# Performance work log

Hardware: AMD Instinct MI355X
Metric: run time of the kernel (lower is better)

The kernel has to match this reference:

```python
import jax, jax.numpy as jnp
import numpy as np

L = 4        # num_layers
B = 32       # batch
N = 512      # num_nodes == seq_len
D = 256      # d_model
H = 8        # nhead
HD = D // H  # head_dim
F = 1024     # dim_feedforward
EPS = 1e-5


def setup_inputs() -> dict:
    key = jax.random.key(0)
    ks = jax.random.split(key, 12)
    w = lambda k, shape: jax.random.normal(k, shape, jnp.float32) * 0.02
    return {
        "src": jax.random.normal(ks[0], (B, N, D), jnp.float32),
        # node embeddings (torch.randn -> std 1)
        "e1": jax.random.normal(ks[1], (N, D), jnp.float32),
        "e2": jax.random.normal(ks[2], (N, D), jnp.float32),
        # per-layer attention projections, stored [L, d_in, d_out]
        "Wq": w(ks[3], (L, D, D)), "bq": jnp.zeros((L, D), jnp.float32),
        "Wk": w(ks[4], (L, D, D)), "bk": jnp.zeros((L, D), jnp.float32),
        "Wv": w(ks[5], (L, D, D)), "bv": jnp.zeros((L, D), jnp.float32),
        "Wo": w(ks[6], (L, D, D)), "bo": jnp.zeros((L, D), jnp.float32),
        # FFN
        "W1": w(ks[7], (L, D, F)), "b1": jnp.zeros((L, F), jnp.float32),
        "W2": w(ks[8], (L, F, D)), "b2": jnp.zeros((L, D), jnp.float32),
        # LayerNorms
        "g1": jnp.ones((L, D), jnp.float32), "be1": jnp.zeros((L, D), jnp.float32),
        "g2": jnp.ones((L, D), jnp.float32), "be2": jnp.zeros((L, D), jnp.float32),
    }


def _layernorm(x, g, b):
    mu = jnp.mean(x, axis=-1, keepdims=True)
    var = jnp.mean(jnp.square(x - mu), axis=-1, keepdims=True)
    return (x - mu) * jax.lax.rsqrt(var + EPS) * g + b


def reference(src, e1, e2, Wq, bq, Wk, bk, Wv, bv, Wo, bo,
              W1, b1, W2, b2, g1, be1, g2, be2):
    # adaptive spatial bias shared across all layers: [N, N]
    bias = jnp.matmul(e1, e2.T)
    scale = 1.0 / jnp.sqrt(jnp.float32(HD))
    x = src
    for l in range(L):
        def heads(t):  # [B,N,D] -> [B,H,N,HD]
            return t.reshape(B, N, H, HD).transpose(0, 2, 1, 3)
        q = heads(x @ Wq[l] + bq[l])
        k = heads(x @ Wk[l] + bk[l])
        v = heads(x @ Wv[l] + bv[l])
        # scores + shared additive bias (broadcast over batch and heads)
        scores = jnp.einsum('bhqd,bhkd->bhqk', q, k) * scale + bias
        attn = jax.nn.softmax(scores, axis=-1)
        o = jnp.einsum('bhqk,bhkd->bhqd', attn, v)
        o = o.transpose(0, 2, 1, 3).reshape(B, N, D) @ Wo[l] + bo[l]
        x = _layernorm(x + o, g1[l], be1[l])
        ff = jax.nn.relu(x @ W1[l] + b1[l]) @ W2[l] + b2[l]
        x = _layernorm(x + ff, g2[l], be2[l])
    return x
```

## Files before the change

kernel.cpp:

```cpp
#include <hip/hip_runtime.h>

typedef __bf16 bf16;
typedef __bf16 v4bf __attribute__((ext_vector_type(4)));
typedef __bf16 v8bf __attribute__((ext_vector_type(8)));
typedef float  v4f  __attribute__((ext_vector_type(4)));
typedef float  v16f __attribute__((ext_vector_type(16)));
typedef unsigned short u16;
typedef u16 v8us __attribute__((ext_vector_type(8)));
typedef unsigned int v4u __attribute__((ext_vector_type(4)));
typedef _Float16 f16;
typedef f16 v4h __attribute__((ext_vector_type(4)));

#define L_ 4
#define B_ 32
#define N_ 512
#define D_ 256
#define H_ 8
#define F_ 1024
#define ROWS (B_*N_)
#define QHSZ ((size_t)B_*H_*N_*32)

__device__ __forceinline__ void gload16(const void* g, void* l) {
  __builtin_amdgcn_global_load_lds((__attribute__((address_space(1))) void*)g,
                                   (__attribute__((address_space(3))) void*)l,
                                   16, 0, 0);
}

__device__ __forceinline__ unsigned pk_bf16(float a, float b) {
  unsigned r;
  asm("v_cvt_pk_bf16_f32 %0, %1, %2" : "=v"(r) : "v"(a), "v"(b));
  return r;
}

#define PLSWAP(a, b) asm volatile("v_permlane32_swap_b32 %0, %1" : "+v"(a), "+v"(b))

#define EXP2(x) __builtin_amdgcn_exp2f(x)

__device__ __forceinline__ unsigned encf(float f) {
  unsigned u = __float_as_uint(f);
  return (u & 0x80000000u) ? ~u : (u | 0x80000000u);
}
__device__ __forceinline__ float decf(unsigned e) {
  unsigned b = (e & 0x80000000u) ? (e & 0x7fffffffu) : ~e;
  return __uint_as_float(b);
}

template <int N> __device__ __forceinline__ void waitvm() {
  if constexpr (N == 0) asm volatile("s_waitcnt vmcnt(0)" ::: "memory");
  else if constexpr (N == 2) asm volatile("s_waitcnt vmcnt(2)" ::: "memory");
  else if constexpr (N == 3) asm volatile("s_waitcnt vmcnt(3)" ::: "memory");
  else if constexpr (N == 4) asm volatile("s_waitcnt vmcnt(4)" ::: "memory");
  else if constexpr (N == 5) asm volatile("s_waitcnt vmcnt(5)" ::: "memory");
  else if constexpr (N == 6) asm volatile("s_waitcnt vmcnt(6)" ::: "memory");
}

__global__ __launch_bounds__(256) void bias_gemm(
    const float* __restrict__ eK, const float* __restrict__ eQ,
    float* __restrict__ biasP, unsigned* __restrict__ mqe) {
  __shared__ float As[32][17];
  __shared__ float Bs[32][17];
  __shared__ float pm[16][32];
  const int tx = threadIdx.x, ty = threadIdx.y;
  const int t = ty * 16 + tx;
  const int lrow = t >> 3, lkq = (t & 7) * 2;
  const int r0 = blockIdx.y * 32, c0 = blockIdx.x * 32;
  float acc[2][2] = {{0.f, 0.f}, {0.f, 0.f}};
  for (int k0 = 0; k0 < D_; k0 += 16) {
    const float2 a2 = *(const float2*)&eK[(size_t)(r0 + lrow) * D_ + k0 + lkq];
    const float2 b2 = *(const float2*)&eQ[(size_t)(c0 + lrow) * D_ + k0 + lkq];
    As[lrow][lkq] = a2.x; As[lrow][lkq + 1] = a2.y;
    Bs[lrow][lkq] = b2.x; Bs[lrow][lkq + 1] = b2.y;
    __syncthreads();
#pragma unroll
    for (int k = 0; k < 16; ++k) {
      const float a0 = As[ty * 2][k], a1 = As[ty * 2 + 1][k];
      const float b0 = Bs[tx * 2][k], b1 = Bs[tx * 2 + 1][k];
      acc[0][0] += a0 * b0; acc[0][1] += a0 * b1;
      acc[1][0] += a1 * b0; acc[1][1] += a1 * b1;
    }
    __syncthreads();
  }
#pragma unroll
  for (int i = 0; i < 2; ++i)
#pragma unroll
    for (int j = 0; j < 2; ++j) acc[i][j] *= 1.4426950408889634f;
#pragma unroll
  for (int i = 0; i < 2; ++i) {
    const int gr = r0 + ty * 2 + i;
    const int kb = gr >> 5, r5 = gr & 31;
    const int blk = kb * 8 + (r5 >> 3) * 2 + ((r5 >> 2) & 1);
#pragma unroll
    for (int j = 0; j < 2; ++j) {
      const int q = c0 + tx * 2 + j;
      biasP[(size_t)(blk * 512 + q) * 4 + (r5 & 3)] = acc[i][j];
    }
  }
  pm[ty][tx * 2]     = fmaxf(acc[0][0], acc[1][0]);
  pm[ty][tx * 2 + 1] = fmaxf(acc[0][1], acc[1][1]);
  __syncthreads();
  if (ty == 0) {
#pragma unroll
    for (int j = 0; j < 2; ++j) {
      float m = pm[0][tx * 2 + j];
#pragma unroll
      for (int y = 1; y < 16; ++y) m = fmaxf(m, pm[y][tx * 2 + j]);
      atomicMax(&mqe[c0 + tx * 2 + j], encf(m));
    }
  }
}

__device__ __forceinline__ void convT_tile(
    const float* __restrict__ W, bf16* __restrict__ Wt,
    int K, int N, size_t inL, size_t outL, int l, int k0, int n0, int tid,
    float (*t)[33]) {
  const int r = tid >> 5, c = tid & 31;
#pragma unroll
  for (int i = 0; i < 4; ++i)
    t[r + 8 * i][c] = W[l * inL + (size_t)(k0 + r + 8 * i) * N + n0 + c];
  __syncthreads();
#pragma unroll
  for (int i = 0; i < 4; ++i)
    Wt[l * outL + (size_t)(n0 + r + 8 * i) * K + k0 + c] = (bf16)t[c][r + 8 * i];
}

__global__ __launch_bounds__(256) void setup_all(
    const float* __restrict__ src, bf16* __restrict__ xb,
    const float* __restrict__ bq, const float* __restrict__ bk,
    const float* __restrict__ bv, float* __restrict__ bqkv,
    const float* __restrict__ Wq, const float* __restrict__ Wk,
    const float* __restrict__ Wv, const float* __restrict__ Wo,
    const float* __restrict__ W1, const float* __restrict__ W2,
    bf16* __restrict__ Wqkvt, bf16* __restrict__ Wot,
    bf16* __restrict__ W1t, bf16* __restrict__ W2t,
    const float* __restrict__ biasP, f16* __restrict__ biasH,
    const unsigned* __restrict__ mqe) {
  __shared__ float t[32][33];
  const int tid = threadIdx.x;
  int id = blockIdx.x;
  if (id < 4096) {
    const int i = id * 256 + tid;
    float4 v = ((const float4*)src)[i];
    uint2 w;
    w.x = pk_bf16(v.x, v.y);
    w.y = pk_bf16(v.z, v.w);
    ((uint2*)xb)[i] = w;
    return;
  }
  id -= 4096;
  if (id < 12) {
    const int i = id * 256 + tid;
    if (i < L_ * 768) {
      const int l = i / 768, n = i - l * 768;
      float v = (n < 256) ? bq[l * 256 + n]
              : (n < 512) ? bk[l * 256 + n - 256]
                          : bv[l * 256 + n - 512];
      bqkv[i] = v;
    }
    return;
  }
  id -= 12;
  if (id < 1024) {
    const int w = id >> 8, tt = id & 255;
    const int l = tt >> 6, tile = tt & 63;
    const int n0 = (tile & 7) * 32, k0 = (tile >> 3) * 32;
    const float* W = (w == 0) ? Wq : (w == 1) ? Wk : (w == 2) ? Wv : Wo;
    bf16* Wt = (w == 3) ? Wot : (Wqkvt + w * 65536);
    const size_t outL = (w == 3) ? 65536 : 196608;
    convT_tile(W, Wt, 256, 256, 65536, outL, l, k0, n0, tid, t);
    return;
  }
  id -= 1024;
  if (id < 1024) {
    const int l = id >> 8, tile = id & 255;
    const int n0 = (tile & 31) * 32, k0 = (tile >> 5) * 32;
    convT_tile(W1, W1t, 256, 1024, 262144, 262144, l, k0, n0, tid, t);
    return;
  }
  id -= 1024;
  if (id < 1024) {
    const int l = id >> 8, tile = id & 255;
    const int n0 = (tile & 7) * 32, k0 = (tile >> 3) * 32;
    convT_tile(W2, W2t, 1024, 256, 262144, 262144, l, k0, n0, tid, t);
    return;
  }
  id -= 1024;
  {
    const int i = id * 256 + tid;
    const float4 v = ((const float4*)biasP)[i];
    const float m = decf(mqe[i & 511]);
    v4h o;
    o[0] = (f16)(v.x - m); o[1] = (f16)(v.y - m);
    o[2] = (f16)(v.z - m); o[3] = (f16)(v.w - m);
    *(v4h*)&biasH[(size_t)i * 4] = o;
  }
}

template <int BM, int BN, int WPC, int RELU, int OUTMODE, int RESID>
__global__ __launch_bounds__(256, WPC) void gemm_bf16k(
    const bf16* __restrict__ A, const bf16* __restrict__ Bt,
    const float* __restrict__ bias, const bf16* __restrict__ resid,
    void* __restrict__ Cout, int M, int N, int K, int nbx) {
  constexpr int MR = BM / 32, NR = BN / 32;
  constexpr int NSLAB = (BM + BN) / 16;
  constexpr int LPW = NSLAB / 4;
  constexpr int BUFE = (BM + BN) * 32;
  __shared__ __align__(16) bf16 lds[3 * BUFE];
  const int tid  = threadIdx.x;
  const int wave = tid >> 6, lane = tid & 63;
  const int l15 = lane & 15, l4 = lane >> 4;
  const int qq = gridDim.x >> 3;
  const int wg = (blockIdx.x & 7) * qq + (blockIdx.x >> 3);
  const int bx = wg % nbx, by = wg / nbx;
  const int bm = by * BM, bn = bx * BN;
  const int wr = (wave >> 1) * (BM / 2), wc = (wave & 1) * (BN / 2);
  const int lrow = lane >> 2;
  const int lk   = (lane & 3) * 8;

  v4f acc[MR][NR];
#pragma unroll
  for (int m = 0; m < MR; ++m)
#pragma unroll
    for (int n = 0; n < NR; ++n) acc[m][n] = (v4f){0.f, 0.f, 0.f, 0.f};

  auto STAGE = [&](int buf, int k0) {
    bf16* dst = &lds[buf * BUFE];
#pragma unroll
    for (int s = wave; s < NSLAB; s += 4) {
      if (s < BM / 16)
        gload16(A + (size_t)(bm + s * 16 + lrow) * K + k0 + lk, dst + s * 512);
      else
        gload16(Bt + (size_t)(bn + (s - BM / 16) * 16 + lrow) * K + k0 + lk, dst + s * 512);
    }
  };

  const int nk = K >> 5;
  STAGE(0, 0);
  STAGE(1, 32);
  waitvm<LPW>();
  __builtin_amdgcn_s_barrier();
  __builtin_amdgcn_sched_barrier(0);

  int cur = 0;
  for (int t = 0; t < nk; ++t) {
    const bool pf = (t + 2 < nk);
    if (pf) STAGE(cur == 0 ? 2 : cur - 1, (t + 2) * 32);
    const bf16* buf = &lds[cur * BUFE];
    v8bf af[MR], bfr[NR];
#pragma unroll
    for (int m = 0; m < MR; ++m)
      af[m] = *(const v8bf*)&buf[(wr + m * 16 + l15) * 32 + l4 * 8];
#pragma unroll
    for (int n = 0; n < NR; ++n)
      bfr[n] = *(const v8bf*)&buf[BM * 32 + (wc + n * 16 + l15) * 32 + l4 * 8];
    __builtin_amdgcn_s_setprio(1);
#pragma unroll
    for (int m = 0; m < MR; ++m)
#pragma unroll
      for (int n = 0; n < NR; ++n)
        acc[m][n] = __builtin_amdgcn_mfma_f32_16x16x32_bf16(af[m], bfr[n], acc[m][n], 0, 0, 0);
    __builtin_amdgcn_s_setprio(0);
    if (pf) waitvm<LPW>();
    else    waitvm<0>();
    __builtin_amdgcn_s_barrier();
    __builtin_amdgcn_sched_barrier(0);
    cur = (cur == 2) ? 0 : cur + 1;
  }

#pragma unroll
  for (int m = 0; m < MR; ++m) {
    const int row0 = bm + wr + m * 16 + l4 * 4;
#pragma unroll
    for (int n = 0; n < NR; ++n) {
      const int col = bn + wc + n * 16 + l15;
      const float bc = bias[col];
      if constexpr (OUTMODE == 2) {
        const int sec = col >> 8, hh = (col >> 5) & 7, d = col & 31;
        const int bb = row0 >> 9, nr0 = row0 & 511;
        bf16* dst = (bf16*)Cout + (size_t)sec * QHSZ +
                    (((size_t)bb * 8 + hh) * 512 + nr0) * 32 + d;
#pragma unroll
        for (int i = 0; i < 4; ++i)
          dst[i * 32] = (bf16)(acc[m][n][i] + bc);
      } else {
#pragma unroll
        for (int i = 0; i < 4; ++i) {
          const size_t idx = (size_t)(row0 + i) * N + col;
          float v = acc[m][n][i] + bc;
          if (RESID) v += (float)resid[idx];
          if (RELU) v = fmaxf(v, 0.f);
          if (OUTMODE == 1) ((bf16*)Cout)[idx] = (bf16)v;
          else              ((float*)Cout)[idx] = v;
        }
      }
    }
  }
}

#define VTS 520
__global__ __launch_bounds__(512, 2) void attn_k(
    const bf16* __restrict__ qkvh, const f16* __restrict__ biasH,
    bf16* __restrict__ outp) {
  __shared__ u16 Vt[32 * VTS];
  const int tid = threadIdx.x;
  const int wave = tid >> 6, lane = tid & 63;
  const int l31 = lane & 31, hi = lane >> 5;
  const int fid = blockIdx.x;
  const int xcd = fid & 7, idx = fid >> 3;
  const int b = (xcd << 2) | (idx >> 4);
  const int h = (idx >> 1) & 7;
  const int qhalf = idx & 1;
  const u16* Qh = (const u16*)qkvh + (((size_t)b * 8 + h) * 512) * 32;
  const u16* Kh = Qh + QHSZ;
  const u16* Vh = Qh + 2 * QHSZ;
  const int qb = qhalf * 256 + wave * 32;

  {
    const u16* p0 = Vh + (size_t)tid * 32;
#pragma unroll
    for (int d0 = 0; d0 < 32; d0 += 8) {
      v8us a = *(const v8us*)(p0 + d0);
#pragma unroll
      for (int j = 0; j < 8; ++j)
        Vt[(d0 + j) * VTS + tid] = a[j];
    }
  }
  __syncthreads();

  const u16* qrow = Qh + (size_t)(qb + l31) * 32;
  const v8bf qf0 = *(const v8bf*)(qrow + hi * 8);
  const v8bf qf1 = *(const v8bf*)(qrow + 16 + hi * 8);
  const f16* bpl = biasH + ((size_t)(hi * 512 + qb + l31)) * 4;

  const float SC2 = 0.17677669529663688f * 1.4426950408889634f;
  float lsum = 0.f;
  v16f accO = {0.f,0.f,0.f,0.f,0.f,0.f,0.f,0.f,0.f,0.f,0.f,0.f,0.f,0.f,0.f,0.f};

  v8bf ka0 = *(const v8bf*)(Kh + (size_t)l31 * 32 + hi * 8);
  v8bf ka1 = *(const v8bf*)(Kh + (size_t)l31 * 32 + 16 + hi * 8);
  v4h bb[4];
#pragma unroll
  for (int g = 0; g < 4; ++g) bb[g] = *(const v4h*)(bpl + (size_t)(g * 2) * 2048);

  v16f stC = {0.f,0.f,0.f,0.f,0.f,0.f,0.f,0.f,0.f,0.f,0.f,0.f,0.f,0.f,0.f,0.f};
  stC = __builtin_amdgcn_mfma_f32_32x32x16_bf16(ka0, qf0, stC, 0, 0, 0);
  stC = __builtin_amdgcn_mfma_f32_32x32x16_bf16(ka1, qf1, stC, 0, 0, 0);
  {
    const u16* kn = Kh + (size_t)(32 + l31) * 32;
    ka0 = *(const v8bf*)(kn + hi * 8);
    ka1 = *(const v8bf*)(kn + 16 + hi * 8);
  }

  for (int kb = 0; kb < 16; ++kb) {
    const int kbase = kb * 32;
    v16f stN = {0.f,0.f,0.f,0.f,0.f,0.f,0.f,0.f,0.f,0.f,0.f,0.f,0.f,0.f,0.f,0.f};
    __builtin_amdgcn_s_setprio(1);
    stN = __builtin_amdgcn_mfma_f32_32x32x16_bf16(ka0, qf0, stN, 0, 0, 0);
    stN = __builtin_amdgcn_mfma_f32_32x32x16_bf16(ka1, qf1, stN, 0, 0, 0);
    __builtin_amdgcn_s_setprio(0);

    const u16* kn = Kh + (size_t)(kbase + 64 + l31) * 32;
    const v8bf kn0 = *(const v8bf*)(kn + hi * 8);
    const v8bf kn1 = *(const v8bf*)(kn + 16 + hi * 8);
    v4h bn[4];
#pragma unroll
    for (int g = 0; g < 4; ++g)
      bn[g] = *(const v4h*)(bpl + (size_t)((kb + 1) * 8 + g * 2) * 2048);

    float p[16];
#pragma unroll
    for (int r = 0; r < 16; ++r)
      p[r] = EXP2(fmaf(stC[r], SC2, (float)bb[r >> 2][r & 3]));

    float s8[8], s4[4];
#pragma unroll
    for (int r = 0; r < 8; ++r) s8[r] = p[r] + p[r + 8];
#pragma unroll
    for (int r = 0; r < 4; ++r) s4[r] = s8[r] + s8[r + 4];
    lsum += (s4[0] + s4[2]) + (s4[1] + s4[3]);

    unsigned u[8];
#pragma unroll
    for (int t = 0; t < 8; ++t) u[t] = pk_bf16(p[2 * t], p[2 * t + 1]);
    PLSWAP(u[0], u[2]);
    PLSWAP(u[1], u[3]);
    PLSWAP(u[4], u[6]);
    PLSWAP(u[5], u[7]);
    union { v4u u; v8bf h; } cv0, cv1;
    cv0.u = (v4u){u[0], u[1], u[2], u[3]};
    cv1.u = (v4u){u[4], u[5], u[6], u[7]};

    const v8bf va0 = *(const v8bf*)&Vt[l31 * VTS + kbase + hi * 8];
    const v8bf va1 = *(const v8bf*)&Vt[l31 * VTS + kbase + 16 + hi * 8];
    __builtin_amdgcn_s_setprio(1);
    accO = __builtin_amdgcn_mfma_f32_32x32x16_bf16(va0, cv0.h, accO, 0, 0, 0);
    accO = __builtin_amdgcn_mfma_f32_32x32x16_bf16(va1, cv1.h, accO, 0, 0, 0);
    __builtin_amdgcn_s_setprio(0);

    stC = stN;
    ka0 = kn0; ka1 = kn1;
#pragma unroll
    for (int g = 0; g < 4; ++g) bb[g] = bn[g];
  }

  lsum += __shfl_xor(lsum, 32);

  const float inv = 1.0f / lsum;
  u16* orow = (u16*)outp + (size_t)(b * N_ + qb + l31) * D_ + h * 32 + 4 * hi;
#pragma unroll
  for (int g = 0; g < 4; ++g) {
    uint2 w;
    w.x = pk_bf16(accO[4 * g] * inv, accO[4 * g + 1] * inv);
    w.y = pk_bf16(accO[4 * g + 2] * inv, accO[4 * g + 3] * inv);
    *(uint2*)(orow + 8 * g) = w;
  }
}

template <int MODE>
__global__ __launch_bounds__(256) void ln_kernel(
    const float* __restrict__ xin,
    const float* __restrict__ g, const float* __restrict__ b,
    float* __restrict__ xout_f32, bf16* __restrict__ xbout) {
  const int wv = threadIdx.x >> 6, ln = threadIdx.x & 63;
  const size_t row = blockIdx.x * 4 + wv;
  const size_t o4 = row * D_ + ln * 4;
  const float4 v = *(const float4*)&xin[o4];
  float s  = (v.x + v.y) + (v.z + v.w);
  float ss = (v.x * v.x + v.y * v.y) + (v.z * v.z + v.w * v.w);
#pragma unroll
  for (int off = 1; off < 64; off <<= 1) {
    s  += __shfl_xor(s, off);
    ss += __shfl_xor(ss, off);
  }
  const float mu = s * (1.f / D_);
  const float var = ss * (1.f / D_) - mu * mu;
  const float rs = rsqrtf(var + 1e-5f);
  const float4 gg = *(const float4*)&g[ln * 4];
  const float4 bb = *(const float4*)&b[ln * 4];
  float4 o;
  o.x = (v.x - mu) * rs * gg.x + bb.x;
  o.y = (v.y - mu) * rs * gg.y + bb.y;
  o.z = (v.z - mu) * rs * gg.z + bb.z;
  o.w = (v.w - mu) * rs * gg.w + bb.w;
  if constexpr (MODE == 1) {
    *(float4*)&xout_f32[o4] = o;
  } else {
    uint2 w;
    w.x = pk_bf16(o.x, o.y);
    w.y = pk_bf16(o.z, o.w);
    *(uint2*)&xbout[o4] = w;
  }
}

extern "C" void kernel_launch(void* const* d_in, const int* in_sizes, int n_in,
                              void* d_out, int out_size, void* d_ws, size_t ws_size,
                              hipStream_t stream) {
  const float* src = (const float*)d_in[0];
  const float* e1  = (const float*)d_in[1];
  const float* e2  = (const float*)d_in[2];
  const float* Wq  = (const float*)d_in[3];
  const float* bq  = (const float*)d_in[4];
  const float* Wk  = (const float*)d_in[5];
  const float* bk  = (const float*)d_in[6];
  const float* Wv  = (const float*)d_in[7];
  const float* bv  = (const float*)d_in[8];
  const float* Wo  = (const float*)d_in[9];
  const float* bo  = (const float*)d_in[10];
  const float* W1  = (const float*)d_in[11];
  const float* b1  = (const float*)d_in[12];
  const float* W2  = (const float*)d_in[13];
  const float* b2  = (const float*)d_in[14];
  const float* g1  = (const float*)d_in[15];
  const float* be1 = (const float*)d_in[16];
  const float* g2  = (const float*)d_in[17];
  const float* be2 = (const float*)d_in[18];

  char* ws = (char*)d_ws;
  size_t off = 0;
  auto alloc = [&](size_t bytes) {
    void* p = ws + off;
    off += (bytes + 255) & ~(size_t)255;
    return p;
  };
  float*    biasP  = (float*)alloc((size_t)1024 * 1024 + 4096);
  f16*      biasH  = (f16*)  alloc((size_t)2 * 1024 * 1024);
  unsigned* mqe    = (unsigned*)alloc((size_t)N_ * 4);
  bf16*     xb     = (bf16*) alloc((size_t)ROWS * D_ * 2);
  bf16*     attn_o = (bf16*) alloc((size_t)ROWS * D_ * 2);
  float*    tmpf   = (float*)alloc((size_t)ROWS * D_ * 4);
  bf16*     qkvh   = (bf16*) alloc((size_t)ROWS * 1024 * 2 + 65536);
  bf16*     h1     = qkvh;
  bf16*     Wqkvt  = (bf16*) alloc((size_t)L_ * 768 * 256 * 2);
  bf16*     Wot    = (bf16*) alloc((size_t)L_ * 256 * 256 * 2);
  bf16*     W1t    = (bf16*) alloc((size_t)L_ * 1024 * 256 * 2);
  bf16*     W2t    = (bf16*) alloc((size_t)L_ * 256 * 1024 * 2);
  float*    bqkv   = (float*)alloc((size_t)L_ * 768 * 4);

  hipMemsetAsync(mqe, 0, (size_t)N_ * 4, stream);
  bias_gemm<<<dim3(16, 16), dim3(16, 16), 0, stream>>>(e2, e1, biasP, mqe);
  setup_all<<<7436, 256, 0, stream>>>(
      src, xb, bq, bk, bv, bqkv,
      Wq, Wk, Wv, Wo, W1, W2, Wqkvt, Wot, W1t, W2t, biasP, biasH, mqe);

  for (int l = 0; l < L_; ++l) {
    gemm_bf16k<128, 128, 3, 0, 2, 0><<<768, 256, 0, stream>>>(
        xb, Wqkvt + (size_t)l * 196608, bqkv + l * 768, nullptr, qkvh,
        ROWS, 768, 256, 6);
    attn_k<<<512, 512, 0, stream>>>(qkvh, biasH, attn_o);
    gemm_bf16k<64, 128, 4, 0, 0, 1><<<512, 256, 0, stream>>>(
        attn_o, Wot + (size_t)l * 65536, bo + l * 256, xb, tmpf,
        ROWS, 256, 256, 2);
    ln_kernel<0><<<ROWS / 4, 256, 0, stream>>>(tmpf, g1 + l * 256, be1 + l * 256, nullptr, xb);
    gemm_bf16k<128, 256, 2, 1, 1, 0><<<512, 256, 0, stream>>>(
        xb, W1t + (size_t)l * 262144, b1 + l * 1024, nullptr, h1,
        ROWS, 1024, 256, 4);
    gemm_bf16k<64, 128, 4, 0, 0, 1><<<512, 256, 0, stream>>>(
        h1, W2t + (size_t)l * 262144, b2 + l * 256, xb, tmpf,
        ROWS, 256, 1024, 2);
    if (l == L_ - 1)
      ln_kernel<1><<<ROWS / 4, 256, 0, stream>>>(tmpf, g2 + l * 256, be2 + l * 256, (float*)d_out, nullptr);
    else
      ln_kernel<0><<<ROWS / 4, 256, 0, stream>>>(tmpf, g2 + l * 256, be2 + l * 256, nullptr, xb);
  }
}
```

Before: 431.5 us.

## Fuse FFN up- and down-projection GEMMs into one kernel keeping hidden in LDS

Replaces the two FFN GEMM launches with a single kernel. Each 64-row block computes the ReLU hidden activations in 128-column chunks, stages them in shared memory, and immediately accumulates the down-projection into register accumulators. This removes the global write and read of the 16384x1024 bf16 hidden tensor and one launch. In exchange, weights are streamed straight from global memory into registers with no LDS tiling, only 256 blocks are launched, and the output tile is fixed at 64x256, so occupancy and weight reuse may be lower than the tuned GEMMs.

```diff
diff --git a/kernel.cpp b/kernel.cpp
--- a/kernel.cpp
+++ b/kernel.cpp
@@ -296,6 +296,132 @@
   }
 }
 
+__global__ __launch_bounds__(256, 2) void ffn_k(
+    const bf16* __restrict__ xb, const bf16* __restrict__ W1t,
+    const float* __restrict__ b1, const bf16* __restrict__ W2t,
+    const float* __restrict__ b2, float* __restrict__ tmpf) {
+  __shared__ __align__(16) bf16 xs[64][264];
+  __shared__ __align__(16) bf16 hs[64][136];
+  const int tid = threadIdx.x;
+  const int wave = tid >> 6, lane = tid & 63;
+  const int l15 = lane & 15, l4 = lane >> 4;
+  const int wg = (blockIdx.x & 7) * 32 + (blockIdx.x >> 3);
+  const int bm = wg * 64;
+  const int wr = (wave >> 1) * 32;
+  const int wc1 = (wave & 1) * 64;
+  const int wc2 = (wave & 1) * 128;
+
+  {
+    const int r = tid >> 2, c0 = (tid & 3) * 64;
+    const bf16* srcp = xb + (size_t)(bm + r) * 256 + c0;
+#pragma unroll
+    for (int j = 0; j < 8; ++j)
+      *(v8bf*)&xs[r][c0 + j * 8] = *(const v8bf*)(srcp + j * 8);
+  }
+  __syncthreads();
+
+  v4f yacc[2][8];
+#pragma unroll
+  for (int m = 0; m < 2; ++m)
+#pragma unroll
+    for (int n = 0; n < 8; ++n) yacc[m][n] = (v4f){0.f, 0.f, 0.f, 0.f};
+
+  for (int nc = 0; nc < 8; ++nc) {
+    const int nb = nc * 128;
+    v4f hacc[2][4];
+#pragma unroll
+    for (int m = 0; m < 2; ++m)
+#pragma unroll
+      for (int n = 0; n < 4; ++n) hacc[m][n] = (v4f){0.f, 0.f, 0.f, 0.f};
+    {
+      const bf16* w1base = W1t + (size_t)(nb + wc1 + l15) * 256 + l4 * 8;
+      v8bf bcur[4];
+#pragma unroll
+      for (int n = 0; n < 4; ++n) bcur[n] = *(const v8bf*)(w1base + (size_t)(n * 16) * 256);
+#pragma unroll
+      for (int ks = 0; ks < 8; ++ks) {
+        v8bf bnext[4];
+        if (ks < 7) {
+#pragma unroll
+          for (int n = 0; n < 4; ++n)
+            bnext[n] = *(const v8bf*)(w1base + (size_t)(n * 16) * 256 + (ks + 1) * 32);
+        }
+        const v8bf a0 = *(const v8bf*)&xs[wr + l15][ks * 32 + l4 * 8];
+        const v8bf a1 = *(const v8bf*)&xs[wr + 16 + l15][ks * 32 + l4 * 8];
+        __builtin_amdgcn_s_setprio(1);
+#pragma unroll
+        for (int n = 0; n < 4; ++n) {
+          hacc[0][n] = __builtin_amdgcn_mfma_f32_16x16x32_bf16(a0, bcur[n], hacc[0][n], 0, 0, 0);
+          hacc[1][n] = __builtin_amdgcn_mfma_f32_16x16x32_bf16(a1, bcur[n], hacc[1][n], 0, 0, 0);
+        }
+        __builtin_amdgcn_s_setprio(0);
+        if (ks < 7) {
+#pragma unroll
+          for (int n = 0; n < 4; ++n) bcur[n] = bnext[n];
+        }
+      }
+    }
+#pragma unroll
+    for (int m = 0; m < 2; ++m)
+#pragma unroll
+      for (int n = 0; n < 4; ++n) {
+        const int col = wc1 + n * 16 + l15;
+        const float bb = b1[nb + col];
+#pragma unroll
+        for (int i = 0; i < 4; ++i) {
+          float h = hacc[m][n][i] + bb;
+          h = fmaxf(h, 0.f);
+          hs[wr + m * 16 + l4 * 4 + i][col] = (bf16)h;
+        }
+      }
+    __syncthreads();
+    {
+      const bf16* w2base = W2t + (size_t)(wc2 + l15) * 1024 + nb + l4 * 8;
+      v8bf bcur[8];
+#pragma unroll
+      for (int n = 0; n < 8; ++n) bcur[n] = *(const v8bf*)(w2base + (size_t)(n * 16) * 1024);
+#pragma unroll
+      for (int ks = 0; ks < 4; ++ks) {
+        v8bf bnext[8];
+        if (ks < 3) {
+#pragma unroll
+          for (int n = 0; n < 8; ++n)
+            bnext[n] = *(const v8bf*)(w2base + (size_t)(n * 16) * 1024 + (ks + 1) * 32);
+        }
+        const v8bf a0 = *(const v8bf*)&hs[wr + l15][ks * 32 + l4 * 8];
+        const v8bf a1 = *(const v8bf*)&hs[wr + 16 + l15][ks * 32 + l4 * 8];
+        __builtin_amdgcn_s_setprio(1);
+#pragma unroll
+        for (int n = 0; n < 8; ++n) {
+          yacc[0][n] = __builtin_amdgcn_mfma_f32_16x16x32_bf16(a0, bcur[n], yacc[0][n], 0, 0, 0);
+          yacc[1][n] = __builtin_amdgcn_mfma_f32_16x16x32_bf16(a1, bcur[n], yacc[1][n], 0, 0, 0);
+        }
+        __builtin_amdgcn_s_setprio(0);
+        if (ks < 3) {
+#pragma unroll
+          for (int n = 0; n < 8; ++n) bcur[n] = bnext[n];
+        }
+      }
+    }
+    __syncthreads();
+  }
+
+#pragma unroll
+  for (int m = 0; m < 2; ++m) {
+    const int row0 = bm + wr + m * 16 + l4 * 4;
+#pragma unroll
+    for (int n = 0; n < 8; ++n) {
+      const int col = wc2 + n * 16 + l15;
+      const float bc = b2[col];
+#pragma unroll
+      for (int i = 0; i < 4; ++i) {
+        const size_t idx = (size_t)(row0 + i) * 256 + col;
+        tmpf[idx] = yacc[m][n][i] + bc + (float)xb[idx];
+      }
+    }
+  }
+}
+
 #define VTS 520
 __global__ __launch_bounds__(512, 2) void attn_k(
     const bf16* __restrict__ qkvh, const f16* __restrict__ biasH,
@@ -487,8 +613,7 @@
   bf16*     xb     = (bf16*) alloc((size_t)ROWS * D_ * 2);
   bf16*     attn_o = (bf16*) alloc((size_t)ROWS * D_ * 2);
   float*    tmpf   = (float*)alloc((size_t)ROWS * D_ * 4);
-  bf16*     qkvh   = (bf16*) alloc((size_t)ROWS * 1024 * 2 + 65536);
-  bf16*     h1     = qkvh;
+  bf16*     qkvh   = (bf16*) alloc((size_t)ROWS * 768 * 2 + 65536);
   bf16*     Wqkvt  = (bf16*) alloc((size_t)L_ * 768 * 256 * 2);
   bf16*     Wot    = (bf16*) alloc((size_t)L_ * 256 * 256 * 2);
   bf16*     W1t    = (bf16*) alloc((size_t)L_ * 1024 * 256 * 2);
@@ -510,12 +635,9 @@
         attn_o, Wot + (size_t)l * 65536, bo + l * 256, xb, tmpf,
         ROWS, 256, 256, 2);
     ln_kernel<0><<<ROWS / 4, 256, 0, stream>>>(tmpf, g1 + l * 256, be1 + l * 256, nullptr, xb);
-    gemm_bf16k<128, 256, 2, 1, 1, 0><<<512, 256, 0, stream>>>(
-        xb, W1t + (size_t)l * 262144, b1 + l * 1024, nullptr, h1,
-        ROWS, 1024, 256, 4);
-    gemm_bf16k<64, 128, 4, 0, 0, 1><<<512, 256, 0, stream>>>(
-        h1, W2t + (size_t)l * 262144, b2 + l * 256, xb, tmpf,
-        ROWS, 256, 1024, 2);
+    ffn_k<<<256, 256, 0, stream>>>(
+        xb, W1t + (size_t)l * 262144, b1 + l * 1024,
+        W2t + (size_t)l * 262144, b2 + l * 256, tmpf);
     if (l == L_ - 1)
       ln_kernel<1><<<ROWS / 4, 256, 0, stream>>>(tmpf, g2 + l * 256, be2 + l * 256, (float*)d_out, nullptr);
     else
```

New measurement: 600.1 us. +39.1%, slower.
